# Kernel optimization log

Hardware: AMD Instinct MI355X
Metric: run time of the kernel (lower is better)

Reference implementation:

```python
import jax, jax.numpy as jnp
import numpy as np
import math

BT, N, D, H = 16, 1024, 128, 8
HD = D // H


def setup_inputs() -> dict:
    key = jax.random.key(0)
    ks = jax.random.split(key, 12)
    s = 1.0 / math.sqrt(D)
    return {
        "x": jax.random.normal(ks[0], (BT, N, D), dtype=jnp.float32),
        "adj": jax.random.uniform(ks[1], (BT, N, N), dtype=jnp.float32),
        "Wq": jax.random.normal(ks[2], (D, D), dtype=jnp.float32) * s,
        "bq": jax.random.normal(ks[3], (D,), dtype=jnp.float32) * 0.01,
        "Wk": jax.random.normal(ks[4], (D, D), dtype=jnp.float32) * s,
        "bk": jax.random.normal(ks[5], (D,), dtype=jnp.float32) * 0.01,
        "Wv": jax.random.normal(ks[6], (D, D), dtype=jnp.float32) * s,
        "bv": jax.random.normal(ks[7], (D,), dtype=jnp.float32) * 0.01,
        "Wo": jax.random.normal(ks[8], (D, D), dtype=jnp.float32) * s,
        "bo": jax.random.normal(ks[9], (D,), dtype=jnp.float32) * 0.01,
    }


def reference(x, adj, Wq, bq, Wk, bk, Wv, bv, Wo, bo):
    bt, n, d = x.shape
    # projections (torch Linear: x @ W.T + b), split into heads -> (BT,H,N,HD)
    q = (x @ Wq.T + bq).reshape(bt, n, H, HD).transpose(0, 2, 1, 3)
    k = (x @ Wk.T + bk).reshape(bt, n, H, HD).transpose(0, 2, 1, 3)
    v = (x @ Wv.T + bv).reshape(bt, n, H, HD).transpose(0, 2, 1, 3)
    scores = jnp.einsum('bhnd,bhmd->bhnm', q, k) / math.sqrt(HD)  # (BT,H,N,N)
    mask = (adj == 0)[:, None, :, :]  # (BT,1,N,N)
    scores = jnp.where(mask, -jnp.inf, scores)
    attn = jax.nn.softmax(scores, axis=-1)
    attn = attn * adj[:, None, :, :]  # reweight by continuous causal strength
    attn = attn / (attn.sum(axis=-1, keepdims=True) + 1e-8)  # renormalize
    ctx = jnp.einsum('bhnm,bhmd->bhnd', attn, v)  # (BT,H,N,HD)
    ctx = ctx.transpose(0, 2, 1, 3).reshape(bt, n, d)
    return ctx @ Wo.T + bo
```

## Files before the change

### kernel.cpp

```cpp
#include <hip/hip_runtime.h>
#include <hip/hip_bf16.h>

#define BTC 16
#define NC 1024
#define DC 128
#define HC 8
#define HDC 16

typedef __attribute__((ext_vector_type(8))) short bf16x8;
typedef __attribute__((ext_vector_type(4))) float f32x4;
typedef __attribute__((ext_vector_type(16))) float f32x16;
typedef __attribute__((ext_vector_type(4))) short short4v;

#if __has_builtin(__builtin_amdgcn_exp2f)
#define EXP2F(x) __builtin_amdgcn_exp2f(x)
#else
#define EXP2F(x) exp2f(x)
#endif

#define QSCALE 0.36067376022224085f

union PK2 { short4v s4; __hip_bfloat162 h2[2]; };
union PK8 { bf16x8 v; short s[8]; __hip_bfloat162 h2[4]; };

static __device__ inline short f2bf(float f) {
    unsigned u = __builtin_bit_cast(unsigned, f);
    u += 0x7fffu + ((u >> 16) & 1u);
    return (short)(u >> 16);
}

#define LDS_BARRIER()                                              \
    do {                                                           \
        asm volatile("s_waitcnt lgkmcnt(0)" ::: "memory");         \
        __builtin_amdgcn_s_barrier();                              \
        asm volatile("" ::: "memory");                             \
    } while (0)

__global__ __launch_bounds__(256)
void prep_kernel(const float* __restrict__ x,
                 const float* __restrict__ Wq, const float* __restrict__ Wk,
                 const float* __restrict__ Wv, const float* __restrict__ Wo,
                 short* __restrict__ xbf, short* __restrict__ Wbf)
{
    int gid  = blockIdx.x * 256 + threadIdx.x;
    int base = gid * 4;
    const float* src;
    short* dst;
    if (base < 2097152) {
        src = x + base; dst = xbf + base;
    } else {
        int idx = base - 2097152;
        int w   = idx >> 14;
        int off = idx & 16383;
        src = ((w == 0) ? Wq : (w == 1) ? Wk : (w == 2) ? Wv : Wo) + off;
        dst = Wbf + w * 16384 + off;
    }
    float4 v = *(const float4*)src;
    PK2 pk;
    pk.h2[0] = __float22bfloat162_rn(make_float2(v.x, v.y));
    pk.h2[1] = __float22bfloat162_rn(make_float2(v.z, v.w));
    *(short4v*)dst = pk.s4;
}

__global__ __launch_bounds__(256)
void proj_qkv(const short* __restrict__ xbf, const short* __restrict__ Wbf,
              const float* __restrict__ bq, const float* __restrict__ bk,
              const float* __restrict__ bv,
              short* __restrict__ qo, short* __restrict__ ko, short* __restrict__ vto)
{
    __shared__ short T[128 * 72];

    const int y = blockIdx.y;
    const short* W = Wbf + y * 16384;
    const float* bias = (y == 0) ? bq : (y == 1) ? bk : bv;
    const float scale = (y == 0) ? QSCALE : 1.0f;

    const int tid  = threadIdx.x;
    const int wave = tid >> 6;
    const int lane = tid & 63;
    const int l15  = lane & 15;
    const int quad = lane >> 4;
    const int rowA = blockIdx.x * 64 + wave * 16;

    f32x4 acc[8];
#pragma unroll
    for (int t = 0; t < 8; ++t) acc[t] = (f32x4){0.f, 0.f, 0.f, 0.f};

#pragma unroll
    for (int kk = 0; kk < DC; kk += 32) {
        bf16x8 Af = *(const bf16x8*)&xbf[(size_t)(rowA + l15) * DC + kk + quad * 8];
#pragma unroll
        for (int t = 0; t < 8; ++t) {
            bf16x8 Bf = *(const bf16x8*)&W[(t * 16 + l15) * DC + kk + quad * 8];
            acc[t] = __builtin_amdgcn_mfma_f32_16x16x32_bf16(Af, Bf, acc[t], 0, 0, 0);
        }
    }

    if (y == 2) {
#pragma unroll
        for (int t = 0; t < 8; ++t) {
            int c = t * 16 + l15;
            float b = bias[c];
            PK2 pk;
            pk.h2[0] = __float22bfloat162_rn(make_float2(acc[t][0] + b, acc[t][1] + b));
            pk.h2[1] = __float22bfloat162_rn(make_float2(acc[t][2] + b, acc[t][3] + b));
            *(short4v*)&T[c * 72 + wave * 16 + quad * 4] = pk.s4;
        }
        __syncthreads();
        const int bt = blockIdx.x >> 4;
        const int n0 = (blockIdx.x * 64) & 1023;
        const int chunk = tid & 7;
        const int dr    = tid >> 3;
#pragma unroll
        for (int rep = 0; rep < 4; ++rep) {
            int d = rep * 32 + dr;
            bf16x8 u = *(const bf16x8*)&T[d * 72 + chunk * 8];
            *(bf16x8*)&vto[((size_t)bt * DC + d) * NC + n0 + chunk * 8] = u;
        }
    } else {
        short* dst = (y == 0) ? qo : ko;
#pragma unroll
        for (int t = 0; t < 8; ++t) {
            int c  = t * 16 + l15;
            int hh = c >> 4, dd = c & 15;
            float b = bias[c];
#pragma unroll
            for (int r = 0; r < 4; ++r) {
                int row = rowA + quad * 4 + r;
                int btq = row >> 10, n = row & 1023;
                float val = (acc[t][r] + b) * scale;
                dst[(((size_t)btq * HC + hh) * NC + n) * HDC + dd] = f2bf(val);
            }
        }
    }
}

__global__ __launch_bounds__(256)
void proj_out(const short* __restrict__ cbf, const short* __restrict__ Wobf,
              const float* __restrict__ bo, float* __restrict__ out)
{
    const int tid  = threadIdx.x;
    const int wave = tid >> 6;
    const int lane = tid & 63;
    const int l15  = lane & 15;
    const int quad = lane >> 4;
    const int rowA = blockIdx.x * 64 + wave * 16;

    f32x4 acc[8];
#pragma unroll
    for (int t = 0; t < 8; ++t) acc[t] = (f32x4){0.f, 0.f, 0.f, 0.f};

#pragma unroll
    for (int kk = 0; kk < DC; kk += 32) {
        bf16x8 Af = *(const bf16x8*)&cbf[(size_t)(rowA + l15) * DC + kk + quad * 8];
#pragma unroll
        for (int t = 0; t < 8; ++t) {
            bf16x8 Bf = *(const bf16x8*)&Wobf[(t * 16 + l15) * DC + kk + quad * 8];
            acc[t] = __builtin_amdgcn_mfma_f32_16x16x32_bf16(Af, Bf, acc[t], 0, 0, 0);
        }
    }

#pragma unroll
    for (int t = 0; t < 8; ++t) {
        int c = t * 16 + l15;
        float b = bo[c];
#pragma unroll
        for (int r = 0; r < 4; ++r) {
            int row = rowA + quad * 4 + r;
            out[(size_t)row * DC + c] = acc[t][r] + b;
        }
    }
}

__global__ __launch_bounds__(256, 4)
void attn_kernel(const short* __restrict__ qh, const short* __restrict__ kh,
                 const short* __restrict__ vt, const float* __restrict__ adj,
                 short* __restrict__ cb)
{
    __shared__ float As[2][32 * 68];
    __shared__ short Ps[4][32 * 72];

    const int tid  = threadIdx.x;
    const int wave = tid >> 6;
    const int lane = tid & 63;
    const int l31  = lane & 31;
    const int hi   = lane >> 5;
    const int l15  = lane & 15;
    const int quad = lane >> 4;
    const int bt   = blockIdx.y;
    const int qt0  = blockIdx.x * 32;
    const int h    = blockIdx.z * 4 + wave;

    const size_t xb = (size_t)bt * NC * DC;
    const size_t hb = ((size_t)bt * HC + h) * NC;

    const short* kp = kh + (hb + l31) * HDC + hi * 8;
    const short* vp = vt + ((size_t)bt * DC + h * HDC + l15) * NC;
    const bf16x8 Bq = *(const bf16x8*)&qh[(hb + qt0 + l31) * HDC + hi * 8];

    const int arow = tid >> 3;
    const int acolf = (tid & 7) * 8;
    const float* aptr = adj + (size_t)bt * NC * NC + (size_t)(qt0 + arow) * NC + acolf;
    const int awoff = arow * 68 + acolf;

    PK8 ones;
#pragma unroll
    for (int j = 0; j < 8; ++j) ones.s[j] = (short)0x3F80;

    f32x16 Z16;
#pragma unroll
    for (int i = 0; i < 16; ++i) Z16[i] = 0.f;

    f32x4 Cc[2], Cw[2];
#pragma unroll
    for (int s = 0; s < 2; ++s) {
        Cc[s] = (f32x4){0.f, 0.f, 0.f, 0.f};
        Cw[s] = (f32x4){0.f, 0.f, 0.f, 0.f};
    }

    short* Pw = &Ps[wave][0];

#define EXPTILE(S, ASB, H2)                                                   \
    do {                                                                      \
        const float* asb = (ASB) + l31 * 68 + (H2) + hi * 4;                  \
        float4 a0 = *(const float4*)&asb[0];                                  \
        float4 a1 = *(const float4*)&asb[8];                                  \
        float4 a2 = *(const float4*)&asb[16];                                 \
        float4 a3 = *(const float4*)&asb[24];                                 \
        short* pd = Pw + l31 * 72 + (H2) + hi * 4;                            \
        PK2 pk;                                                               \
        pk.h2[0] = __float22bfloat162_rn(                                     \
            make_float2(EXP2F(S[0]) * a0.x, EXP2F(S[1]) * a0.y));             \
        pk.h2[1] = __float22bfloat162_rn(                                     \
            make_float2(EXP2F(S[2]) * a0.z, EXP2F(S[3]) * a0.w));             \
        *(short4v*)&pd[0] = pk.s4;                                            \
        pk.h2[0] = __float22bfloat162_rn(                                     \
            make_float2(EXP2F(S[4]) * a1.x, EXP2F(S[5]) * a1.y));             \
        pk.h2[1] = __float22bfloat162_rn(                                     \
            make_float2(EXP2F(S[6]) * a1.z, EXP2F(S[7]) * a1.w));             \
        *(short4v*)&pd[8] = pk.s4;                                            \
        pk.h2[0] = __float22bfloat162_rn(                                     \
            make_float2(EXP2F(S[8]) * a2.x, EXP2F(S[9]) * a2.y));             \
        pk.h2[1] = __float22bfloat162_rn(                                     \
            make_float2(EXP2F(S[10]) * a2.z, EXP2F(S[11]) * a2.w));           \
        *(short4v*)&pd[16] = pk.s4;                                           \
        pk.h2[0] = __float22bfloat162_rn(                                     \
            make_float2(EXP2F(S[12]) * a3.x, EXP2F(S[13]) * a3.y));           \
        pk.h2[1] = __float22bfloat162_rn(                                     \
            make_float2(EXP2F(S[14]) * a3.z, EXP2F(S[15]) * a3.w));           \
        *(short4v*)&pd[24] = pk.s4;                                           \
    } while (0)

    float4 p0a = *(const float4*)&aptr[0];
    float4 p0b = *(const float4*)&aptr[4];
    float4 ara = *(const float4*)&aptr[64];
    float4 arb = *(const float4*)&aptr[68];
    bf16x8 AkA = *(const bf16x8*)&kp[0];
    bf16x8 AkB = *(const bf16x8*)&kp[32 * HDC];

    *(float4*)((char*)&As[0][0] + awoff * 4)      = p0a;
    *(float4*)((char*)&As[0][0] + awoff * 4 + 16) = p0b;
    LDS_BARRIER();

    {
        float4 arna = *(const float4*)&aptr[128];
        float4 arnb = *(const float4*)&aptr[132];
        bf16x8 AkAn = *(const bf16x8*)&kp[64 * HDC];
        bf16x8 AkBn = *(const bf16x8*)&kp[96 * HDC];

        f32x16 S0 = __builtin_amdgcn_mfma_f32_32x32x16_bf16(AkA, Bq, Z16, 0, 0, 0);
        EXPTILE(S0, &As[0][0], 0);
        f32x16 S1 = __builtin_amdgcn_mfma_f32_32x32x16_bf16(AkB, Bq, Z16, 0, 0, 0);
        EXPTILE(S1, &As[0][0], 32);

        *(float4*)((char*)&As[1][0] + awoff * 4)      = ara;
        *(float4*)((char*)&As[1][0] + awoff * 4 + 16) = arb;
        LDS_BARRIER();

        ara = arna; arb = arnb; AkA = AkAn; AkB = AkBn;
    }

    for (int it = 1; it < 16; ++it) {
        const int jt  = it * 64;
        const int cur = it & 1;

        bf16x8 ApA0 = *(const bf16x8*)&Pw[l15 * 72 + quad * 8];
        bf16x8 ApA1 = *(const bf16x8*)&Pw[(16 + l15) * 72 + quad * 8];
        bf16x8 ApB0 = *(const bf16x8*)&Pw[l15 * 72 + 32 + quad * 8];
        bf16x8 ApB1 = *(const bf16x8*)&Pw[(16 + l15) * 72 + 32 + quad * 8];
        bf16x8 BvpA = *(const bf16x8*)&vp[jt - 64 + quad * 8];
        bf16x8 BvpB = *(const bf16x8*)&vp[jt - 32 + quad * 8];
        const int nj2 = (jt + 128) & (NC - 1);
        float4 arna = *(const float4*)&aptr[nj2];
        float4 arnb = *(const float4*)&aptr[nj2 + 4];
        bf16x8 AkAn = *(const bf16x8*)&kp[((jt + 64) & (NC - 1)) * HDC];
        bf16x8 AkBn = *(const bf16x8*)&kp[((jt + 96) & (NC - 1)) * HDC];

        f32x16 S0 = __builtin_amdgcn_mfma_f32_32x32x16_bf16(AkA, Bq, Z16, 0, 0, 0);

        __builtin_amdgcn_s_setprio(1);
        Cc[0] = __builtin_amdgcn_mfma_f32_16x16x32_bf16(ApA0, BvpA, Cc[0], 0, 0, 0);
        Cw[0] = __builtin_amdgcn_mfma_f32_16x16x32_bf16(ApA0, ones.v, Cw[0], 0, 0, 0);
        Cc[1] = __builtin_amdgcn_mfma_f32_16x16x32_bf16(ApA1, BvpA, Cc[1], 0, 0, 0);
        Cw[1] = __builtin_amdgcn_mfma_f32_16x16x32_bf16(ApA1, ones.v, Cw[1], 0, 0, 0);
        Cc[0] = __builtin_amdgcn_mfma_f32_16x16x32_bf16(ApB0, BvpB, Cc[0], 0, 0, 0);
        Cw[0] = __builtin_amdgcn_mfma_f32_16x16x32_bf16(ApB0, ones.v, Cw[0], 0, 0, 0);
        Cc[1] = __builtin_amdgcn_mfma_f32_16x16x32_bf16(ApB1, BvpB, Cc[1], 0, 0, 0);
        Cw[1] = __builtin_amdgcn_mfma_f32_16x16x32_bf16(ApB1, ones.v, Cw[1], 0, 0, 0);
        __builtin_amdgcn_s_setprio(0);

        EXPTILE(S0, &As[cur][0], 0);
        f32x16 S1 = __builtin_amdgcn_mfma_f32_32x32x16_bf16(AkB, Bq, Z16, 0, 0, 0);
        EXPTILE(S1, &As[cur][0], 32);

        *(float4*)((char*)&As[cur ^ 1][0] + awoff * 4)      = ara;
        *(float4*)((char*)&As[cur ^ 1][0] + awoff * 4 + 16) = arb;
        LDS_BARRIER();

        ara = arna; arb = arnb; AkA = AkAn; AkB = AkBn;
    }

    {
        bf16x8 ApA0 = *(const bf16x8*)&Pw[l15 * 72 + quad * 8];
        bf16x8 ApA1 = *(const bf16x8*)&Pw[(16 + l15) * 72 + quad * 8];
        bf16x8 ApB0 = *(const bf16x8*)&Pw[l15 * 72 + 32 + quad * 8];
        bf16x8 ApB1 = *(const bf16x8*)&Pw[(16 + l15) * 72 + 32 + quad * 8];
        bf16x8 BvpA = *(const bf16x8*)&vp[960 + quad * 8];
        bf16x8 BvpB = *(const bf16x8*)&vp[992 + quad * 8];
        Cc[0] = __builtin_amdgcn_mfma_f32_16x16x32_bf16(ApA0, BvpA, Cc[0], 0, 0, 0);
        Cw[0] = __builtin_amdgcn_mfma_f32_16x16x32_bf16(ApA0, ones.v, Cw[0], 0, 0, 0);
        Cc[1] = __builtin_amdgcn_mfma_f32_16x16x32_bf16(ApA1, BvpA, Cc[1], 0, 0, 0);
        Cw[1] = __builtin_amdgcn_mfma_f32_16x16x32_bf16(ApA1, ones.v, Cw[1], 0, 0, 0);
        Cc[0] = __builtin_amdgcn_mfma_f32_16x16x32_bf16(ApB0, BvpB, Cc[0], 0, 0, 0);
        Cw[0] = __builtin_amdgcn_mfma_f32_16x16x32_bf16(ApB0, ones.v, Cw[0], 0, 0, 0);
        Cc[1] = __builtin_amdgcn_mfma_f32_16x16x32_bf16(ApB1, BvpB, Cc[1], 0, 0, 0);
        Cw[1] = __builtin_amdgcn_mfma_f32_16x16x32_bf16(ApB1, ones.v, Cw[1], 0, 0, 0);
    }

#pragma unroll
    for (int s = 0; s < 2; ++s)
#pragma unroll
        for (int r = 0; r < 4; ++r) {
            float den = Cw[s][r];
            float rcp = den > 0.f ? 1.f / den : 0.f;
            int row = qt0 + s * 16 + quad * 4 + r;
            cb[xb + (size_t)row * DC + h * HDC + l15] = f2bf(Cc[s][r] * rcp);
        }
#undef EXPTILE
}

extern "C" void kernel_launch(void* const* d_in, const int* in_sizes, int n_in,
                              void* d_out, int out_size, void* d_ws, size_t ws_size,
                              hipStream_t stream)
{
    const float* x   = (const float*)d_in[0];
    const float* adj = (const float*)d_in[1];
    const float* Wq  = (const float*)d_in[2];
    const float* bq  = (const float*)d_in[3];
    const float* Wk  = (const float*)d_in[4];
    const float* bk  = (const float*)d_in[5];
    const float* Wv  = (const float*)d_in[6];
    const float* bv  = (const float*)d_in[7];
    const float* Wo  = (const float*)d_in[8];
    const float* bo  = (const float*)d_in[9];
    float* out = (float*)d_out;

    const size_t tok = (size_t)BTC * NC * DC;
    short* xbf  = (short*)d_ws;
    short* Wbf  = xbf  + tok;
    short* qbuf = Wbf  + 65536;
    short* kbuf = qbuf + tok;
    short* vt   = kbuf + tok;
    short* cbuf = vt   + tok;

    prep_kernel<<<2112, 256, 0, stream>>>(x, Wq, Wk, Wv, Wo, xbf, Wbf);

    dim3 pgrid(256, 3);
    proj_qkv<<<pgrid, 256, 0, stream>>>(xbf, Wbf, bq, bk, bv, qbuf, kbuf, vt);

    dim3 agrid(32, 16, 2);
    attn_kernel<<<agrid, 256, 0, stream>>>(qbuf, kbuf, vt, adj, cbuf);

    proj_out<<<256, 256, 0, stream>>>(cbuf, Wbf + 3 * 16384, bo, out);
}
```

Baseline: 169.6 us.

## Swizzle LDS tiles and prefetch P/V operands one iteration ahead

Replaces the padded LDS layouts for the adjacency and probability tiles with unpadded XOR-swizzled layouts, which shrinks shared memory and is meant to avoid bank conflicts. The P-tile LDS reads move to just before the barrier of the previous iteration, and the V loads are issued one iteration ahead, so the PV MFMAs no longer wait on fresh loads at the top of the loop. The trade-off is more live registers across the barrier, which could hurt occupancy or cause spills.

```diff
diff --git a/kernel.cpp b/kernel.cpp
--- a/kernel.cpp
+++ b/kernel.cpp
@@ -177,8 +177,8 @@
                  const short* __restrict__ vt, const float* __restrict__ adj,
                  short* __restrict__ cb)
 {
-    __shared__ float As[2][32 * 68];
-    __shared__ short Ps[4][32 * 72];
+    __shared__ float As[2][32 * 64];
+    __shared__ short Ps[4][32 * 64];
 
     const int tid  = threadIdx.x;
     const int wave = tid >> 6;
@@ -199,9 +199,12 @@
     const bf16x8 Bq = *(const bf16x8*)&qh[(hb + qt0 + l31) * HDC + hi * 8];
 
     const int arow = tid >> 3;
-    const int acolf = (tid & 7) * 8;
-    const float* aptr = adj + (size_t)bt * NC * NC + (size_t)(qt0 + arow) * NC + acolf;
-    const int awoff = arow * 68 + acolf;
+    const float* aptr = adj + (size_t)bt * NC * NC + (size_t)(qt0 + arow) * NC
+                        + (tid & 7) * 8;
+    const unsigned awz = (unsigned)((arow & 7) << 4);
+    const unsigned wo  = (unsigned)(arow * 256 + (tid & 7) * 32);
+    const unsigned swz = (unsigned)((l31 & 7) << 4);
+    const unsigned pswz = (unsigned)((l15 & 7) << 4);
 
     PK8 ones;
 #pragma unroll
@@ -218,38 +221,50 @@
         Cw[s] = (f32x4){0.f, 0.f, 0.f, 0.f};
     }
 
-    short* Pw = &Ps[wave][0];
+    char* Pw = (char*)&Ps[wave][0];
 
 #define EXPTILE(S, ASB, H2)                                                   \
     do {                                                                      \
-        const float* asb = (ASB) + l31 * 68 + (H2) + hi * 4;                  \
-        float4 a0 = *(const float4*)&asb[0];                                  \
-        float4 a1 = *(const float4*)&asb[8];                                  \
-        float4 a2 = *(const float4*)&asb[16];                                 \
-        float4 a3 = *(const float4*)&asb[24];                                 \
-        short* pd = Pw + l31 * 72 + (H2) + hi * 4;                            \
+        const char* asb = (const char*)(ASB);                                 \
+        const unsigned ro = (unsigned)(l31 * 256 + (H2) * 4 + hi * 16);       \
+        float4 a0 = *(const float4*)(asb + ((ro +  0) ^ swz));                \
+        float4 a1 = *(const float4*)(asb + ((ro + 32) ^ swz));                \
+        float4 a2 = *(const float4*)(asb + ((ro + 64) ^ swz));                \
+        float4 a3 = *(const float4*)(asb + ((ro + 96) ^ swz));                \
+        const unsigned po = (unsigned)(l31 * 128 + (H2) * 2 + hi * 8);        \
         PK2 pk;                                                               \
         pk.h2[0] = __float22bfloat162_rn(                                     \
             make_float2(EXP2F(S[0]) * a0.x, EXP2F(S[1]) * a0.y));             \
         pk.h2[1] = __float22bfloat162_rn(                                     \
             make_float2(EXP2F(S[2]) * a0.z, EXP2F(S[3]) * a0.w));             \
-        *(short4v*)&pd[0] = pk.s4;                                            \
+        *(short4v*)(Pw + ((po +  0) ^ swz)) = pk.s4;                          \
         pk.h2[0] = __float22bfloat162_rn(                                     \
             make_float2(EXP2F(S[4]) * a1.x, EXP2F(S[5]) * a1.y));             \
         pk.h2[1] = __float22bfloat162_rn(                                     \
             make_float2(EXP2F(S[6]) * a1.z, EXP2F(S[7]) * a1.w));             \
-        *(short4v*)&pd[8] = pk.s4;                                            \
+        *(short4v*)(Pw + ((po + 16) ^ swz)) = pk.s4;                          \
         pk.h2[0] = __float22bfloat162_rn(                                     \
             make_float2(EXP2F(S[8]) * a2.x, EXP2F(S[9]) * a2.y));             \
         pk.h2[1] = __float22bfloat162_rn(                                     \
             make_float2(EXP2F(S[10]) * a2.z, EXP2F(S[11]) * a2.w));           \
-        *(short4v*)&pd[16] = pk.s4;                                           \
+        *(short4v*)(Pw + ((po + 32) ^ swz)) = pk.s4;                          \
         pk.h2[0] = __float22bfloat162_rn(                                     \
             make_float2(EXP2F(S[12]) * a3.x, EXP2F(S[13]) * a3.y));           \
         pk.h2[1] = __float22bfloat162_rn(                                     \
             make_float2(EXP2F(S[14]) * a3.z, EXP2F(S[15]) * a3.w));           \
-        *(short4v*)&pd[24] = pk.s4;                                           \
+        *(short4v*)(Pw + ((po + 48) ^ swz)) = pk.s4;                          \
     } while (0)
+
+#define PREADS(A0, A1, B0, B1)                                                \
+    do {                                                                      \
+        const unsigned q16 = (unsigned)(quad * 16);                           \
+        A0 = *(const bf16x8*)(Pw + (((unsigned)(l15 * 128) + q16) ^ pswz));   \
+        A1 = *(const bf16x8*)(Pw + (((unsigned)((16 + l15) * 128) + q16) ^ pswz)); \
+        B0 = *(const bf16x8*)(Pw + (((unsigned)(l15 * 128 + 64) + q16) ^ pswz));   \
+        B1 = *(const bf16x8*)(Pw + (((unsigned)((16 + l15) * 128 + 64) + q16) ^ pswz)); \
+    } while (0)
+
+    bf16x8 ApA0, ApA1, ApB0, ApB1;
 
     float4 p0a = *(const float4*)&aptr[0];
     float4 p0b = *(const float4*)&aptr[4];
@@ -257,9 +272,11 @@
     float4 arb = *(const float4*)&aptr[68];
     bf16x8 AkA = *(const bf16x8*)&kp[0];
     bf16x8 AkB = *(const bf16x8*)&kp[32 * HDC];
-
-    *(float4*)((char*)&As[0][0] + awoff * 4)      = p0a;
-    *(float4*)((char*)&As[0][0] + awoff * 4 + 16) = p0b;
+    bf16x8 BvpA = *(const bf16x8*)&vp[quad * 8];
+    bf16x8 BvpB = *(const bf16x8*)&vp[32 + quad * 8];
+
+    *(float4*)((char*)&As[0][0] + ((wo)      ^ awz)) = p0a;
+    *(float4*)((char*)&As[0][0] + ((wo + 16) ^ awz)) = p0b;
     LDS_BARRIER();
 
     {
@@ -273,8 +290,10 @@
         f32x16 S1 = __builtin_amdgcn_mfma_f32_32x32x16_bf16(AkB, Bq, Z16, 0, 0, 0);
         EXPTILE(S1, &As[0][0], 32);
 
-        *(float4*)((char*)&As[1][0] + awoff * 4)      = ara;
-        *(float4*)((char*)&As[1][0] + awoff * 4 + 16) = arb;
+        PREADS(ApA0, ApA1, ApB0, ApB1);
+
+        *(float4*)((char*)&As[1][0] + ((wo)      ^ awz)) = ara;
+        *(float4*)((char*)&As[1][0] + ((wo + 16) ^ awz)) = arb;
         LDS_BARRIER();
 
         ara = arna; arb = arnb; AkA = AkAn; AkB = AkBn;
@@ -284,12 +303,8 @@
         const int jt  = it * 64;
         const int cur = it & 1;
 
-        bf16x8 ApA0 = *(const bf16x8*)&Pw[l15 * 72 + quad * 8];
-        bf16x8 ApA1 = *(const bf16x8*)&Pw[(16 + l15) * 72 + quad * 8];
-        bf16x8 ApB0 = *(const bf16x8*)&Pw[l15 * 72 + 32 + quad * 8];
-        bf16x8 ApB1 = *(const bf16x8*)&Pw[(16 + l15) * 72 + 32 + quad * 8];
-        bf16x8 BvpA = *(const bf16x8*)&vp[jt - 64 + quad * 8];
-        bf16x8 BvpB = *(const bf16x8*)&vp[jt - 32 + quad * 8];
+        bf16x8 BvA = *(const bf16x8*)&vp[jt + quad * 8];
+        bf16x8 BvB = *(const bf16x8*)&vp[jt + 32 + quad * 8];
         const int nj2 = (jt + 128) & (NC - 1);
         float4 arna = *(const float4*)&aptr[nj2];
         float4 arnb = *(const float4*)&aptr[nj2 + 4];
@@ -313,20 +328,17 @@
         f32x16 S1 = __builtin_amdgcn_mfma_f32_32x32x16_bf16(AkB, Bq, Z16, 0, 0, 0);
         EXPTILE(S1, &As[cur][0], 32);
 
-        *(float4*)((char*)&As[cur ^ 1][0] + awoff * 4)      = ara;
-        *(float4*)((char*)&As[cur ^ 1][0] + awoff * 4 + 16) = arb;
+        PREADS(ApA0, ApA1, ApB0, ApB1);
+
+        *(float4*)((char*)&As[cur ^ 1][0] + ((wo)      ^ awz)) = ara;
+        *(float4*)((char*)&As[cur ^ 1][0] + ((wo + 16) ^ awz)) = arb;
         LDS_BARRIER();
 
         ara = arna; arb = arnb; AkA = AkAn; AkB = AkBn;
+        BvpA = BvA; BvpB = BvB;
     }
 
     {
-        bf16x8 ApA0 = *(const bf16x8*)&Pw[l15 * 72 + quad * 8];
-        bf16x8 ApA1 = *(const bf16x8*)&Pw[(16 + l15) * 72 + quad * 8];
-        bf16x8 ApB0 = *(const bf16x8*)&Pw[l15 * 72 + 32 + quad * 8];
-        bf16x8 ApB1 = *(const bf16x8*)&Pw[(16 + l15) * 72 + 32 + quad * 8];
-        bf16x8 BvpA = *(const bf16x8*)&vp[960 + quad * 8];
-        bf16x8 BvpB = *(const bf16x8*)&vp[992 + quad * 8];
         Cc[0] = __builtin_amdgcn_mfma_f32_16x16x32_bf16(ApA0, BvpA, Cc[0], 0, 0, 0);
         Cw[0] = __builtin_amdgcn_mfma_f32_16x16x32_bf16(ApA0, ones.v, Cw[0], 0, 0, 0);
         Cc[1] = __builtin_amdgcn_mfma_f32_16x16x32_bf16(ApA1, BvpA, Cc[1], 0, 0, 0);
@@ -347,6 +359,7 @@
             cb[xb + (size_t)row * DC + h * HDC + l15] = f2bf(Cc[s][r] * rcp);
         }
 #undef EXPTILE
+#undef PREADS
 }
 
 extern "C" void kernel_launch(void* const* d_in, const int* in_sizes, int n_in,
```

After: 175.7 us. 3.6% more time.
